# Kernel tuning notes

Measured on AMD Instinct MI355X. Metric: run time of the kernel, lower is better.

## Reference

```python
import jax, jax.numpy as jnp
import numpy as np

A_BITS = 8
W_BITS = 8
STRIDE = 1
PADDING = 1


def _quant_dequant(t, bits):
    """Symmetric per-tensor min-max quantize-dequantize to `bits` bits.

    This is the math the PCILT lookup-table conv realizes: every LUT entry is
    (quantized activation level) * (quantized weight level), so summing LUT
    entries over the conv window == conv(x_qdq, w_qdq).
    """
    qmax = 2.0 ** (bits - 1) - 1.0
    scale = jnp.maximum(jnp.max(jnp.abs(t)) / qmax, 1e-8)
    return jnp.clip(jnp.round(t / scale), -qmax, qmax) * scale


def setup_inputs() -> dict:
    key = jax.random.key(0)
    k1, k2 = jax.random.split(key)
    x = jax.random.normal(k1, (16, 64, 112, 112), dtype=jnp.float32)  # NCHW
    W = jax.random.normal(k2, (128, 64, 3, 3), dtype=jnp.float32) * 0.05  # OIHW
    return {"x": x, "W": W}


def reference(x, W):
    xq = _quant_dequant(x, A_BITS)
    wq = _quant_dequant(W, W_BITS)
    out = jax.lax.conv_general_dilated(
        xq, wq,
        window_strides=(STRIDE, STRIDE),
        padding=[(PADDING, PADDING), (PADDING, PADDING)],
        dimension_numbers=("NCHW", "OIHW", "NCHW"))
    return out  # [16, 128, 112, 112]
```

## Files before the change

### kernel.cpp

```cpp
#include <hip/hip_runtime.h>
#include <hip/hip_bf16.h>


typedef __attribute__((ext_vector_type(8))) short short8;
typedef __attribute__((ext_vector_type(4))) int   int4v;
typedef __attribute__((ext_vector_type(4))) float f32x4;
typedef __attribute__((ext_vector_type(4))) float float4v;
typedef __attribute__((ext_vector_type(8)))  signed char char8;
typedef __attribute__((ext_vector_type(16))) signed char char16;

#define N_IMG 16
#define C_IN 64
#define HW 112
#define O_CH 128
#define WPITCH 576
#define XPITCH 80
#define TP 72
#define NPART 3136

__global__ __launch_bounds__(256) void absmax_part(const float* __restrict__ x,
                                                   const float* __restrict__ w,
                                                   float* __restrict__ part) {
    const int b = blockIdx.x, tid = threadIdx.x;
    const float4v* x4 = (const float4v*)x;
    const long base = (long)b * 1024 + tid;
    const float4v v0 = x4[base];
    const float4v v1 = x4[base + 256];
    const float4v v2 = x4[base + 512];
    const float4v v3 = x4[base + 768];
    float mx = fmaxf(fmaxf(fmaxf(fabsf(v0.x), fabsf(v0.y)), fmaxf(fabsf(v0.z), fabsf(v0.w))),
                     fmaxf(fmaxf(fabsf(v1.x), fabsf(v1.y)), fmaxf(fabsf(v1.z), fabsf(v1.w))));
    mx = fmaxf(mx, fmaxf(fmaxf(fabsf(v2.x), fabsf(v2.y)), fmaxf(fabsf(v2.z), fabsf(v2.w))));
    mx = fmaxf(mx, fmaxf(fmaxf(fabsf(v3.x), fabsf(v3.y)), fmaxf(fabsf(v3.z), fabsf(v3.w))));
    float mw = 0.f;
    if (b < 72) {
        const float4v q = ((const float4v*)w)[b * 256 + tid];
        mw = fmaxf(fmaxf(fabsf(q.x), fabsf(q.y)), fmaxf(fabsf(q.z), fabsf(q.w)));
    }
    #pragma unroll
    for (int off = 32; off > 0; off >>= 1) {
        mx = fmaxf(mx, __shfl_down(mx, off));
        mw = fmaxf(mw, __shfl_down(mw, off));
    }
    __shared__ float smx[4], smw[4];
    const int wave = tid >> 6, lane = tid & 63;
    if (lane == 0) { smx[wave] = mx; smw[wave] = mw; }
    __syncthreads();
    if (tid == 0) {
        part[b]         = fmaxf(fmaxf(smx[0], smx[1]), fmaxf(smx[2], smx[3]));
        part[NPART + b] = fmaxf(fmaxf(smw[0], smw[1]), fmaxf(smw[2], smw[3]));
    }
}

__global__ __launch_bounds__(256) void quant_wx(const float* __restrict__ x,
                                                const float* __restrict__ w,
                                                const float* __restrict__ part,
                                                unsigned* __restrict__ scal,
                                                signed char* __restrict__ wt8,
                                                signed char* __restrict__ xq8) {
    __shared__ __align__(16) short tile[HW * TP];
    __shared__ float smx[4], smw[4];
    const int tid = threadIdx.x;
    const int wave = tid >> 6, lane = tid & 63;

    float mx = 0.f, mw = 0.f;
    #pragma unroll
    for (int i = 0; i < 13; ++i) {
        const int idx = i * 256 + tid;
        if (idx < NPART) mx = fmaxf(mx, part[idx]);
    }
    if (tid < 72) mw = part[NPART + tid];
    #pragma unroll
    for (int off = 32; off > 0; off >>= 1) {
        mx = fmaxf(mx, __shfl_down(mx, off));
        mw = fmaxf(mw, __shfl_down(mw, off));
    }
    if (lane == 0) { smx[wave] = mx; smw[wave] = mw; }
    __syncthreads();
    const float xm = fmaxf(fmaxf(smx[0], smx[1]), fmaxf(smx[2], smx[3]));
    const float wm = fmaxf(fmaxf(smw[0], smw[1]), fmaxf(smw[2], smw[3]));
    const float sx = fmaxf(xm * (1.f / 127.f), 1e-8f);
    const float sw = fmaxf(wm * (1.f / 127.f), 1e-8f);
    if (blockIdx.x == 0 && tid == 0) {
        scal[0] = __float_as_uint(xm);
        scal[1] = __float_as_uint(wm);
    }

    if (blockIdx.x < 288) {
        const int idx = blockIdx.x * 256 + tid;
        const int kw = idx % 3;
        int t = idx / 3;
        const int kh = t % 3;
        t /= 3;
        const int c = t % C_IN;
        const int o = t / C_IN;
        float v = rintf(w[idx] / sw);
        v = fminf(fmaxf(v, -127.f), 127.f);
        wt8[o * WPITCH + (kh * 3 + kw) * C_IN + c] = (signed char)(int)v;
    }

    const int n = blockIdx.x / HW, h = blockIdx.x % HW;
    const float inv_sx = 1.f / sx;
    #pragma unroll
    for (int i = 0; i < 7; ++i) {
        const int l = i * 256 + tid;
        const int c = l / 28, w4 = l - c * 28;
        const float4v v = *(const float4v*)(x + ((long)(n * C_IN + c) * HW + h) * HW + w4 * 4);
        float q[4];
        q[0] = fminf(fmaxf(rintf(v.x * inv_sx), -127.f), 127.f);
        q[1] = fminf(fmaxf(rintf(v.y * inv_sx), -127.f), 127.f);
        q[2] = fminf(fmaxf(rintf(v.z * inv_sx), -127.f), 127.f);
        q[3] = fminf(fmaxf(rintf(v.w * inv_sx), -127.f), 127.f);
        const int osw = ((c >> 3) ^ (w4 & 7)) * 8 + (c & 7);
        #pragma unroll
        for (int j = 0; j < 4; ++j)
            tile[(w4 * 4 + j) * TP + osw] = (short)q[j];
    }
    __syncthreads();
    const int g = tid & 3, wi = tid >> 2;
    signed char* dst = xq8 + (long)(n * HW + h) * HW * C_IN;
    #pragma unroll
    for (int j = 0; j < 2; ++j) {
        const int ww = j * 64 + wi;
        if (ww < HW) {
            const int sw2 = (ww >> 2) & 7;
            const short8 s0 = *(const short8*)(tile + ww * TP + ((2 * g) ^ sw2) * 8);
            const short8 s1 = *(const short8*)(tile + ww * TP + ((2 * g + 1) ^ sw2) * 8);
            const char8 c0 = __builtin_convertvector(s0, char8);
            const char8 c1 = __builtin_convertvector(s1, char8);
            const char16 cc = __builtin_shufflevector(c0, c1,
                0, 1, 2, 3, 4, 5, 6, 7, 8, 9, 10, 11, 12, 13, 14, 15);
            *(char16*)(dst + ww * C_IN + g * 16) = cc;
        }
    }
}

__global__ __launch_bounds__(256, 4) void conv_kernel(const signed char* __restrict__ xq8,
                                                      const signed char* __restrict__ wt8,
                                                      const unsigned* __restrict__ scal,
                                                      float* __restrict__ out) {
    __shared__ __align__(16) signed char xs[4 * 114 * XPITCH];
    const int tid = threadIdx.x;
    const int wave = tid >> 6, lane = tid & 63;
    const int quad = lane >> 4, l16 = lane & 15;
    const int lin = (blockIdx.x & 7) * 112 + (blockIdx.x >> 3);
    const int n = lin / 56, oh0 = (lin % 56) * 2;

    if (tid < 32) {
        const int r = tid >> 3, col = (tid >> 2) & 1, c16 = tid & 3;
        *(int4v*)(xs + (r * 114 + col * 113) * XPITCH + c16 * 16) = (int4v)0;
    }
    #pragma unroll
    for (int it = 0; it < 7; ++it) {
        const int gph = it * 256 + tid;
        const int r = gph / 448, rem = gph - r * 448;
        const int ow = rem >> 2, c16 = rem & 3;
        const int ih = oh0 - 1 + r;
        int4v v = (int4v)0;
        if ((unsigned)ih < (unsigned)HW)
            v = *(const int4v*)(xq8 + ((long)(n * HW + ih) * HW + ow) * C_IN + c16 * 16);
        *(int4v*)(xs + (r * 114 + ow + 1) * XPITCH + c16 * 16) = v;
    }

    const signed char* wrow0 = wt8 + (wave * 32 + l16) * WPITCH + quad * 16;
    const signed char* wrow1 = wrow0 + 16 * WPITCH;
    const float s = fmaxf(__uint_as_float(scal[0]) * (1.f / 127.f), 1e-8f) *
                    fmaxf(__uint_as_float(scal[1]) * (1.f / 127.f), 1e-8f);

    __syncthreads();

    #pragma unroll
    for (int p = 0; p < 2; ++p) {
        int4v acc[7][2];
        #pragma unroll
        for (int mt = 0; mt < 7; ++mt) { acc[mt][0] = (int4v)0; acc[mt][1] = (int4v)0; }

        int4v bcur0 = *(const int4v*)(wrow0);
        int4v bcur1 = *(const int4v*)(wrow1);
        int4v bnxt0, bnxt1;

        #pragma unroll
        for (int tap = 0; tap < 9; ++tap) {
            if (tap < 8) {
                bnxt0 = *(const int4v*)(wrow0 + (tap + 1) * C_IN);
                bnxt1 = *(const int4v*)(wrow1 + (tap + 1) * C_IN);
            }
            const signed char* rowb = xs + ((p + tap / 3) * 114 + (tap % 3) + l16) * XPITCH + quad * 16;
            #pragma unroll
            for (int mt = 0; mt < 7; ++mt) {
                const int4v afr = *(const int4v*)(rowb + mt * (16 * XPITCH));
                acc[mt][0] = __builtin_amdgcn_mfma_i32_16x16x64_i8(afr, bcur0, acc[mt][0], 0, 0, 0);
                acc[mt][1] = __builtin_amdgcn_mfma_i32_16x16x64_i8(afr, bcur1, acc[mt][1], 0, 0, 0);
            }
            bcur0 = bnxt0;
            bcur1 = bnxt1;
        }

        const int oh = oh0 + p;
        #pragma unroll
        for (int mt = 0; mt < 7; ++mt) {
            #pragma unroll
            for (int ot = 0; ot < 2; ++ot) {
                const int o = wave * 32 + ot * 16 + l16;
                const int mrow = mt * 16 + quad * 4;
                const f32x4 v = __builtin_convertvector(acc[mt][ot], f32x4) * s;
                *(f32x4*)(out + (((long)(n * O_CH + o) * HW + oh) * HW + mrow)) = v;
            }
        }
    }
}

extern "C" void kernel_launch(void* const* d_in, const int* in_sizes, int n_in,
                              void* d_out, int out_size, void* d_ws, size_t ws_size,
                              hipStream_t stream) {
    const float* x = (const float*)d_in[0];
    const float* W = (const float*)d_in[1];
    float* out = (float*)d_out;

    unsigned* scal = (unsigned*)d_ws;
    signed char* wt8 = (signed char*)((char*)d_ws + 1024);
    signed char* xq8 = (signed char*)((char*)d_ws + 76800);
    float* part = (float*)out;

    hipLaunchKernelGGL(absmax_part, dim3(NPART), dim3(256), 0, stream, x, W, part);
    hipLaunchKernelGGL(quant_wx, dim3(N_IMG * HW), dim3(256), 0, stream,
                       x, W, part, scal, wt8, xq8);
    hipLaunchKernelGGL(conv_kernel, dim3(896), dim3(256), 0, stream, xq8, wt8, scal, out);
}
```

Before: 168.8 us.

## Fuse activation quantization into conv kernel, drop int8 intermediate buffer

Moves the quantization of activations into the conv kernel. Each block now reads its four fp32 input rows directly, quantizes them through a shared-memory transpose tile and writes int8 straight into its LDS tile. This removes the global write and re-read of the int8 activation tensor, and weight quantization becomes its own small kernel. In exchange each input row is read and quantized about twice (the row halo overlaps between blocks), LDS use per block grows, and occupancy drops to 3 blocks per CU.

```diff
diff --git a/kernel.cpp b/kernel.cpp
--- a/kernel.cpp
+++ b/kernel.cpp
@@ -1,5 +1,4 @@
 #include <hip/hip_runtime.h>
-#include <hip/hip_bf16.h>
 
 
 typedef __attribute__((ext_vector_type(8))) short short8;
@@ -52,16 +51,46 @@
     }
 }
 
-__global__ __launch_bounds__(256) void quant_wx(const float* __restrict__ x,
-                                                const float* __restrict__ w,
-                                                const float* __restrict__ part,
-                                                unsigned* __restrict__ scal,
-                                                signed char* __restrict__ wt8,
-                                                signed char* __restrict__ xq8) {
+__global__ __launch_bounds__(256) void quant_w_k(const float* __restrict__ w,
+                                                 const float* __restrict__ part,
+                                                 signed char* __restrict__ wt8) {
+    const int tid = threadIdx.x;
+    const int wave = tid >> 6, lane = tid & 63;
+    float mw = (tid < 72) ? part[NPART + tid] : 0.f;
+    #pragma unroll
+    for (int off = 32; off > 0; off >>= 1)
+        mw = fmaxf(mw, __shfl_down(mw, off));
+    __shared__ float smw[4];
+    if (lane == 0) smw[wave] = mw;
+    __syncthreads();
+    const float wm = fmaxf(fmaxf(smw[0], smw[1]), fmaxf(smw[2], smw[3]));
+    const float sw = fmaxf(wm * (1.f / 127.f), 1e-8f);
+
+    const int idx = blockIdx.x * 256 + tid;
+    const int kw = idx % 3;
+    int t = idx / 3;
+    const int kh = t % 3;
+    t /= 3;
+    const int c = t % C_IN;
+    const int o = t / C_IN;
+    float v = rintf(w[idx] / sw);
+    v = fminf(fmaxf(v, -127.f), 127.f);
+    wt8[o * WPITCH + (kh * 3 + kw) * C_IN + c] = (signed char)(int)v;
+}
+
+__global__ __launch_bounds__(256, 3) void conv_fused(const float* __restrict__ x,
+                                                     const float* __restrict__ part,
+                                                     const signed char* __restrict__ wt8,
+                                                     float* __restrict__ out) {
+    __shared__ __align__(16) signed char xs[4 * 114 * XPITCH];
     __shared__ __align__(16) short tile[HW * TP];
     __shared__ float smx[4], smw[4];
     const int tid = threadIdx.x;
     const int wave = tid >> 6, lane = tid & 63;
+    const int quad = lane >> 4, l16 = lane & 15;
+    const int g = tid & 3, wi = tid >> 2;
+    const int lin = (blockIdx.x & 7) * 112 + (blockIdx.x >> 3);
+    const int n = lin / 56, oh0 = (lin % 56) * 2;
 
     float mx = 0.f, mw = 0.f;
     #pragma unroll
@@ -81,93 +110,54 @@
     const float wm = fmaxf(fmaxf(smw[0], smw[1]), fmaxf(smw[2], smw[3]));
     const float sx = fmaxf(xm * (1.f / 127.f), 1e-8f);
     const float sw = fmaxf(wm * (1.f / 127.f), 1e-8f);
-    if (blockIdx.x == 0 && tid == 0) {
-        scal[0] = __float_as_uint(xm);
-        scal[1] = __float_as_uint(wm);
-    }
-
-    if (blockIdx.x < 288) {
-        const int idx = blockIdx.x * 256 + tid;
-        const int kw = idx % 3;
-        int t = idx / 3;
-        const int kh = t % 3;
-        t /= 3;
-        const int c = t % C_IN;
-        const int o = t / C_IN;
-        float v = rintf(w[idx] / sw);
-        v = fminf(fmaxf(v, -127.f), 127.f);
-        wt8[o * WPITCH + (kh * 3 + kw) * C_IN + c] = (signed char)(int)v;
-    }
-
-    const int n = blockIdx.x / HW, h = blockIdx.x % HW;
+    const float s_deq = sx * sw;
     const float inv_sx = 1.f / sx;
-    #pragma unroll
-    for (int i = 0; i < 7; ++i) {
-        const int l = i * 256 + tid;
-        const int c = l / 28, w4 = l - c * 28;
-        const float4v v = *(const float4v*)(x + ((long)(n * C_IN + c) * HW + h) * HW + w4 * 4);
-        float q[4];
-        q[0] = fminf(fmaxf(rintf(v.x * inv_sx), -127.f), 127.f);
-        q[1] = fminf(fmaxf(rintf(v.y * inv_sx), -127.f), 127.f);
-        q[2] = fminf(fmaxf(rintf(v.z * inv_sx), -127.f), 127.f);
-        q[3] = fminf(fmaxf(rintf(v.w * inv_sx), -127.f), 127.f);
-        const int osw = ((c >> 3) ^ (w4 & 7)) * 8 + (c & 7);
-        #pragma unroll
-        for (int j = 0; j < 4; ++j)
-            tile[(w4 * 4 + j) * TP + osw] = (short)q[j];
-    }
-    __syncthreads();
-    const int g = tid & 3, wi = tid >> 2;
-    signed char* dst = xq8 + (long)(n * HW + h) * HW * C_IN;
-    #pragma unroll
-    for (int j = 0; j < 2; ++j) {
-        const int ww = j * 64 + wi;
-        if (ww < HW) {
-            const int sw2 = (ww >> 2) & 7;
-            const short8 s0 = *(const short8*)(tile + ww * TP + ((2 * g) ^ sw2) * 8);
-            const short8 s1 = *(const short8*)(tile + ww * TP + ((2 * g + 1) ^ sw2) * 8);
-            const char8 c0 = __builtin_convertvector(s0, char8);
-            const char8 c1 = __builtin_convertvector(s1, char8);
-            const char16 cc = __builtin_shufflevector(c0, c1,
-                0, 1, 2, 3, 4, 5, 6, 7, 8, 9, 10, 11, 12, 13, 14, 15);
-            *(char16*)(dst + ww * C_IN + g * 16) = cc;
-        }
-    }
-}
-
-__global__ __launch_bounds__(256, 4) void conv_kernel(const signed char* __restrict__ xq8,
-                                                      const signed char* __restrict__ wt8,
-                                                      const unsigned* __restrict__ scal,
-                                                      float* __restrict__ out) {
-    __shared__ __align__(16) signed char xs[4 * 114 * XPITCH];
-    const int tid = threadIdx.x;
-    const int wave = tid >> 6, lane = tid & 63;
-    const int quad = lane >> 4, l16 = lane & 15;
-    const int lin = (blockIdx.x & 7) * 112 + (blockIdx.x >> 3);
-    const int n = lin / 56, oh0 = (lin % 56) * 2;
 
     if (tid < 32) {
         const int r = tid >> 3, col = (tid >> 2) & 1, c16 = tid & 3;
         *(int4v*)(xs + (r * 114 + col * 113) * XPITCH + c16 * 16) = (int4v)0;
     }
-    #pragma unroll
-    for (int it = 0; it < 7; ++it) {
-        const int gph = it * 256 + tid;
-        const int r = gph / 448, rem = gph - r * 448;
-        const int ow = rem >> 2, c16 = rem & 3;
-        const int ih = oh0 - 1 + r;
-        int4v v = (int4v)0;
-        if ((unsigned)ih < (unsigned)HW)
-            v = *(const int4v*)(xq8 + ((long)(n * HW + ih) * HW + ow) * C_IN + c16 * 16);
-        *(int4v*)(xs + (r * 114 + ow + 1) * XPITCH + c16 * 16) = v;
+
+    for (int wr = 0; wr < 4; ++wr) {
+        const int ih = oh0 - 1 + wr;
+        const bool valid = (unsigned)ih < (unsigned)HW;
+        #pragma unroll
+        for (int i = 0; i < 7; ++i) {
+            const int l = i * 256 + tid;
+            const int c = l / 28, w4 = l - c * 28;
+            float4v v = (float4v)0;
+            if (valid)
+                v = *(const float4v*)(x + ((long)(n * C_IN + c) * HW + ih) * HW + w4 * 4);
+            float q[4];
+            q[0] = fminf(fmaxf(rintf(v.x * inv_sx), -127.f), 127.f);
+            q[1] = fminf(fmaxf(rintf(v.y * inv_sx), -127.f), 127.f);
+            q[2] = fminf(fmaxf(rintf(v.z * inv_sx), -127.f), 127.f);
+            q[3] = fminf(fmaxf(rintf(v.w * inv_sx), -127.f), 127.f);
+            const int osw = ((c >> 3) ^ (w4 & 7)) * 8 + (c & 7);
+            #pragma unroll
+            for (int j = 0; j < 4; ++j)
+                tile[(w4 * 4 + j) * TP + osw] = (short)q[j];
+        }
+        __syncthreads();
+        #pragma unroll
+        for (int j = 0; j < 2; ++j) {
+            const int ww = j * 64 + wi;
+            if (ww < HW) {
+                const int sw2 = (ww >> 2) & 7;
+                const short8 s0 = *(const short8*)(tile + ww * TP + ((2 * g) ^ sw2) * 8);
+                const short8 s1 = *(const short8*)(tile + ww * TP + ((2 * g + 1) ^ sw2) * 8);
+                const char8 c0 = __builtin_convertvector(s0, char8);
+                const char8 c1 = __builtin_convertvector(s1, char8);
+                const char16 cc = __builtin_shufflevector(c0, c1,
+                    0, 1, 2, 3, 4, 5, 6, 7, 8, 9, 10, 11, 12, 13, 14, 15);
+                *(char16*)(xs + (wr * 114 + ww + 1) * XPITCH + g * 16) = cc;
+            }
+        }
+        __syncthreads();
     }
 
     const signed char* wrow0 = wt8 + (wave * 32 + l16) * WPITCH + quad * 16;
     const signed char* wrow1 = wrow0 + 16 * WPITCH;
-    const float s = fmaxf(__uint_as_float(scal[0]) * (1.f / 127.f), 1e-8f) *
-                    fmaxf(__uint_as_float(scal[1]) * (1.f / 127.f), 1e-8f);
-
-    __syncthreads();
 
     #pragma unroll
     for (int p = 0; p < 2; ++p) {
@@ -203,7 +193,7 @@
             for (int ot = 0; ot < 2; ++ot) {
                 const int o = wave * 32 + ot * 16 + l16;
                 const int mrow = mt * 16 + quad * 4;
-                const f32x4 v = __builtin_convertvector(acc[mt][ot], f32x4) * s;
+                const f32x4 v = __builtin_convertvector(acc[mt][ot], f32x4) * s_deq;
                 *(f32x4*)(out + (((long)(n * O_CH + o) * HW + oh) * HW + mrow)) = v;
             }
         }
@@ -217,13 +207,10 @@
     const float* W = (const float*)d_in[1];
     float* out = (float*)d_out;
 
-    unsigned* scal = (unsigned*)d_ws;
-    signed char* wt8 = (signed char*)((char*)d_ws + 1024);
-    signed char* xq8 = (signed char*)((char*)d_ws + 76800);
-    float* part = (float*)out;
+    float* part = (float*)((char*)d_ws + 1024);
+    signed char* wt8 = (signed char*)((char*)d_ws + 32768);
 
     hipLaunchKernelGGL(absmax_part, dim3(NPART), dim3(256), 0, stream, x, W, part);
-    hipLaunchKernelGGL(quant_wx, dim3(N_IMG * HW), dim3(256), 0, stream,
-                       x, W, part, scal, wt8, xq8);
-    hipLaunchKernelGGL(conv_kernel, dim3(896), dim3(256), 0, stream, xq8, wt8, scal, out);
-}
+    hipLaunchKernelGGL(quant_w_k, dim3(288), dim3(256), 0, stream, W, part, wt8);
+    hipLaunchKernelGGL(conv_fused, dim3(896), dim3(256), 0, stream, x, part, wt8, out);
+}
```

Measured after the change: 175.0 us. 3.7% more time.
